# Optimization experiments

Measured on AMD Instinct MI355X. Metric: run time of the kernel, lower is better.

The kernel has to match this reference:

```python
import jax, jax.numpy as jnp
import numpy as np

B, T, D, H = 8, 2048, 1024, 128

def setup_inputs() -> dict:
    key = jax.random.key(0)
    ks = jax.random.split(key, 8)
    s = 1.0 / np.sqrt(D)
    return {
        "x": jax.random.normal(ks[0], (B, T, D), dtype=jnp.float32),
        "att": jax.random.normal(ks[1], (B, T, D), dtype=jnp.float32),
        "Wk": jax.random.uniform(ks[2], (D, H), minval=-s, maxval=s, dtype=jnp.float32),
        "bk": jax.random.uniform(ks[3], (H,), minval=-s, maxval=s, dtype=jnp.float32),
        "Wq": jax.random.uniform(ks[4], (D, H), minval=-s, maxval=s, dtype=jnp.float32),
        "bq": jax.random.uniform(ks[5], (H,), minval=-s, maxval=s, dtype=jnp.float32),
        "Wv": jax.random.uniform(ks[6], (D, H), minval=-s, maxval=s, dtype=jnp.float32),
        "bv": jax.random.uniform(ks[7], (H,), minval=-s, maxval=s, dtype=jnp.float32),
    }

def reference(x, att, Wk, bk, Wq, bq, Wv, bv):
    # k, q from `att`; v from `x` (as in the original module)
    k = jnp.einsum('btd,dh->bth', att, Wk) + bk   # [B,T,H]
    q = jnp.einsum('btd,dh->bth', att, Wq) + bq   # [B,T,H]
    v = jnp.einsum('btd,dh->bth', x, Wv) + bv     # [B,T,H]
    # Faithful to source: scores / head_size**(-0.5) == scores * sqrt(head_size)
    scale = jnp.asarray(k.shape[-1], jnp.float32) ** 0.5
    scores = jnp.einsum('bqh,bkh->bqk', q, k) * scale  # [B,T,T]
    att_mat = jax.nn.softmax(scores, axis=-1)
    # dropout p=0.0 -> identity (eval semantics)
    return jnp.einsum('bqk,bkh->bqh', att_mat, v)      # [B,T,H]
```

## Files before the change

### kernel.cpp

```cpp
#include <hip/hip_runtime.h>
#include <stdint.h>

typedef unsigned short u16;
typedef __attribute__((ext_vector_type(8))) short bf16x8;
typedef __attribute__((ext_vector_type(4))) float f32x4;

#define T_LEN 2048
#define D_DIM 1024
#define H_DIM 128
#define SCALE_LOG2 16.32223116f

#define EXP2F(x) __builtin_amdgcn_exp2f(x)

__device__ __forceinline__ u16 f2bf(float f) {
  uint32_t u = __float_as_uint(f);
  u += 0x7FFFu + ((u >> 16) & 1u);
  return (u16)(u >> 16);
}
__device__ __forceinline__ float bf2f(u16 h) { return __uint_as_float(((uint32_t)h) << 16); }

__device__ __forceinline__ void gload16(const void* g, void* l) {
  __builtin_amdgcn_global_load_lds(
      (const __attribute__((address_space(1))) uint32_t*)(uintptr_t)g,
      (__attribute__((address_space(3))) uint32_t*)(uint32_t)(uintptr_t)l,
      16, 0, 0);
}

#define MFMA(a, b, c) __builtin_amdgcn_mfma_f32_16x16x32_bf16((a), (b), (c), 0, 0, 0)

__global__ __launch_bounds__(256) void prep_w(
    const float* __restrict__ Wk, const float* __restrict__ Wq, const float* __restrict__ Wv,
    u16* __restrict__ wqh, u16* __restrict__ wql,
    u16* __restrict__ wkh, u16* __restrict__ wkl,
    u16* __restrict__ wvh) {
  __shared__ u16 th[3][128][16];
  __shared__ u16 tl[2][128][16];
  const int i = threadIdx.x;
  const int d0 = blockIdx.x * 16;
  const int dl = i >> 4;
  const int hb = (i & 15) * 8;
  const int d = d0 + dl;
#pragma unroll
  for (int e = 0; e < 8; ++e) {
    int h = hb + e;
    float q = Wq[d * H_DIM + h] * SCALE_LOG2;
    float k = Wk[d * H_DIM + h];
    float v = Wv[d * H_DIM + h];
    u16 qh = f2bf(q); th[0][h][dl] = qh; tl[0][h][dl] = f2bf(q - bf2f(qh));
    u16 kh = f2bf(k); th[1][h][dl] = kh; tl[1][h][dl] = f2bf(k - bf2f(kh));
    th[2][h][dl] = f2bf(v);
  }
  __syncthreads();
  const int h = i >> 1, c = i & 1;
  u16* planes[5] = {wqh, wql, wkh, wkl, wvh};
  const u16* srcs[5] = {&th[0][0][0], &tl[0][0][0], &th[1][0][0], &tl[1][0][0], &th[2][0][0]};
#pragma unroll
  for (int p = 0; p < 5; ++p) {
    bf16x8 v8 = *(const bf16x8*)(srcs[p] + h * 16 + c * 8);
    *(bf16x8*)(planes[p] + h * 1024 + d0 + c * 8) = v8;
  }
}

__global__ __launch_bounds__(256) void qkv_proj(
    const float* __restrict__ att, const float* __restrict__ x,
    const u16* __restrict__ wqh, const u16* __restrict__ wql,
    const u16* __restrict__ wkh, const u16* __restrict__ wkl,
    const u16* __restrict__ wvh,
    const float* __restrict__ bq, const float* __restrict__ bk, const float* __restrict__ bv,
    u16* __restrict__ qhp, u16* __restrict__ qlp,
    u16* __restrict__ khp, u16* __restrict__ klp,
    u16* __restrict__ vtp) {
  __shared__ __attribute__((aligned(128))) char lds[52 * 1024];
  char* aAh = lds;
  char* aAl = lds + 4096;
  char* aXh = lds + 8192;
  char* wt  = lds + 12288;
  char* vbuf = lds + 12288;

  const int tid = threadIdx.x;
  const int wid = tid >> 6;
  const int ln = tid & 63;
  const int g = ln >> 4;
  const int cl = ln & 15;
  const int t0g = blockIdx.x * 64;

  const f32x4 fz = {0.f, 0.f, 0.f, 0.f};
  f32x4 accq[2][4], acck[2][4], accv[2][4];
#pragma unroll
  for (int a = 0; a < 2; ++a)
#pragma unroll
    for (int s = 0; s < 4; ++s) { accq[a][s] = fz; acck[a][s] = fz; accv[a][s] = fz; }

  const int arow = tid >> 2;
  const int ac = tid & 3;
  const float* attp = att + (size_t)(t0g + arow) * D_DIM + ac * 8;
  const float* xp   = x   + (size_t)(t0g + arow) * D_DIM + ac * 8;
  char* aw = aAh + arow * 64 + ((ac ^ ((arow >> 1) & 3)) * 16);

  for (int ks = 0; ks < 32; ++ks) {
    __syncthreads();
    {
      f32x4 f0 = *(const f32x4*)(attp + ks * 32);
      f32x4 f1 = *(const f32x4*)(attp + ks * 32 + 4);
      f32x4 g0 = *(const f32x4*)(xp + ks * 32);
      f32x4 g1 = *(const f32x4*)(xp + ks * 32 + 4);
      bf16x8 vh, vl, vx;
#pragma unroll
      for (int e = 0; e < 4; ++e) {
        u16 h0 = f2bf(f0[e]); vh[e] = (short)h0; vl[e] = (short)f2bf(f0[e] - bf2f(h0));
        u16 h1 = f2bf(f1[e]); vh[e + 4] = (short)h1; vl[e + 4] = (short)f2bf(f1[e] - bf2f(h1));
        vx[e] = (short)f2bf(g0[e]); vx[e + 4] = (short)f2bf(g1[e]);
      }
      *(bf16x8*)aw = vh;
      *(bf16x8*)(aw + 4096) = vl;
      *(bf16x8*)(aw + 8192) = vx;
    }
#pragma unroll
    for (int j = 0; j < 10; ++j) {
      int seg = wid * 10 + j;
      int p = seg >> 3;
      int s = seg & 7;
      int db = s * 1024 + ln * 16;
      int row = db >> 6;
      int c = (db >> 4) & 3;
      int cs = c ^ ((row >> 1) & 3);
      const u16* wp = (p == 0) ? wqh : (p == 1) ? wql : (p == 2) ? wkh : (p == 3) ? wkl : wvh;
      gload16(wp + row * 1024 + ks * 32 + cs * 8, wt + p * 8192 + s * 1024);
    }
    __syncthreads();
    bf16x8 ah[4], al[4], xh[4];
#pragma unroll
    for (int s = 0; s < 4; ++s) {
      int row = s * 16 + cl;
      int byte = row * 64 + ((g ^ ((row >> 1) & 3)) * 16);
      ah[s] = *(const bf16x8*)(aAh + byte);
      al[s] = *(const bf16x8*)(aAl + byte);
      xh[s] = *(const bf16x8*)(aXh + byte);
    }
#pragma unroll
    for (int lnt = 0; lnt < 2; ++lnt) {
      int hrow = (2 * wid + lnt) * 16 + cl;
      int wb = hrow * 64 + ((g ^ ((hrow >> 1) & 3)) * 16);
      bf16x8 bqh_ = *(const bf16x8*)(wt + 0 * 8192 + wb);
      bf16x8 bql_ = *(const bf16x8*)(wt + 1 * 8192 + wb);
      bf16x8 bkh_ = *(const bf16x8*)(wt + 2 * 8192 + wb);
      bf16x8 bkl_ = *(const bf16x8*)(wt + 3 * 8192 + wb);
      bf16x8 bvh_ = *(const bf16x8*)(wt + 4 * 8192 + wb);
#pragma unroll
      for (int s = 0; s < 4; ++s) {
        accq[lnt][s] = MFMA(ah[s], bqh_, accq[lnt][s]);
        accq[lnt][s] = MFMA(al[s], bqh_, accq[lnt][s]);
        accq[lnt][s] = MFMA(ah[s], bql_, accq[lnt][s]);
        acck[lnt][s] = MFMA(ah[s], bkh_, acck[lnt][s]);
        acck[lnt][s] = MFMA(al[s], bkh_, acck[lnt][s]);
        acck[lnt][s] = MFMA(ah[s], bkl_, acck[lnt][s]);
        accv[lnt][s] = MFMA(xh[s], bvh_, accv[lnt][s]);
      }
    }
  }
  __syncthreads();
#pragma unroll
  for (int lnt = 0; lnt < 2; ++lnt) {
    int h = (2 * wid + lnt) * 16 + cl;
    float bqv = bq[h] * SCALE_LOG2, bkv = bk[h], bvv = bv[h];
#pragma unroll
    for (int s = 0; s < 4; ++s) {
#pragma unroll
      for (int r = 0; r < 4; ++r) {
        int t = s * 16 + g * 4 + r;
        size_t idx = (size_t)(t0g + t) * H_DIM + h;
        float qv = accq[lnt][s][r] + bqv;
        u16 qh_ = f2bf(qv);
        qhp[idx] = qh_;
        qlp[idx] = f2bf(qv - bf2f(qh_));
        float kv = acck[lnt][s][r] + bkv;
        u16 kh_ = f2bf(kv);
        khp[idx] = kh_;
        klp[idx] = f2bf(kv - bf2f(kh_));
        float vv = accv[lnt][s][r] + bvv;
        int c3 = t >> 3;
        int byte = h * 128 + ((c3 ^ (h & 7)) * 16) + (t & 7) * 2;
        *(u16*)(vbuf + byte) = f2bf(vv);
      }
    }
  }
  __syncthreads();
  {
    int h = tid >> 1, half = tid & 1;
    int b_ = t0g >> 11;
    int tb = t0g & 2047;
    u16* dst = vtp + ((size_t)(b_ * H_DIM + h)) * T_LEN + tb + half * 32;
#pragma unroll
    for (int c2 = 0; c2 < 4; ++c2) {
      int c3 = half * 4 + c2;
      bf16x8 v8 = *(const bf16x8*)(vbuf + h * 128 + ((c3 ^ (h & 7)) * 16));
      *(bf16x8*)(dst + c2 * 8) = v8;
    }
  }
}

__global__ __launch_bounds__(256) void attn(
    const u16* __restrict__ qhp, const u16* __restrict__ qlp,
    const u16* __restrict__ khp, const u16* __restrict__ klp,
    const u16* __restrict__ vtp,
    float* __restrict__ out) {
  __shared__ __attribute__((aligned(128))) char lds[56 * 1024];
  char* kH = lds;
  char* kL = lds + 16384;
  char* vT = lds + 32768;
  char* pB = lds + 49152;

  const int tid = threadIdx.x;
  const int wid = tid >> 6;
  const int ln = tid & 63;
  const int g = ln >> 4;
  const int cl = ln & 15;
  const int b_ = blockIdx.y;
  const int t0 = blockIdx.x * 64;
  char* pW = pB + wid * 2048;

  bf16x8 qh_f[4], ql_f[4];
  {
    size_t qrow = (size_t)(b_ * T_LEN + t0 + wid * 16 + cl) * H_DIM;
#pragma unroll
    for (int kc = 0; kc < 4; ++kc) {
      qh_f[kc] = *(const bf16x8*)(qhp + qrow + kc * 32 + g * 8);
      ql_f[kc] = *(const bf16x8*)(qlp + qrow + kc * 32 + g * 8);
    }
  }
  const f32x4 fz = {0.f, 0.f, 0.f, 0.f};
  float m_[4] = {-1e30f, -1e30f, -1e30f, -1e30f};
  float l_[4] = {0.f, 0.f, 0.f, 0.f};
  f32x4 o_[8];
#pragma unroll
  for (int ht = 0; ht < 8; ++ht) o_[ht] = fz;

  for (int kv = 0; kv < 32; ++kv) {
    const int tk = kv * 64;
    __syncthreads();
#pragma unroll
    for (int j = 0; j < 4; ++j) {
      int s = wid * 4 + j;
      int db = s * 1024 + ln * 16;
      int row = db >> 8;
      int c16 = (db >> 4) & 15;
      int cs = c16 ^ (row & 7);
      size_t gidx = (size_t)(b_ * T_LEN + tk + row) * H_DIM + cs * 8;
      gload16(khp + gidx, kH + s * 1024);
      gload16(klp + gidx, kL + s * 1024);
      int vrow = db >> 7;
      int c3 = (db >> 4) & 7;
      int vcs = c3 ^ (vrow & 7);
      size_t vidx = (size_t)(b_ * H_DIM + vrow) * T_LEN + tk + vcs * 8;
      gload16(vtp + vidx, vT + s * 1024);
    }
    __syncthreads();
    f32x4 sc[4];
#pragma unroll
    for (int nt = 0; nt < 4; ++nt) sc[nt] = fz;
#pragma unroll
    for (int kc = 0; kc < 4; ++kc) {
#pragma unroll
      for (int nt = 0; nt < 4; ++nt) {
        int row = nt * 16 + cl;
        int byte = row * 256 + (((kc * 4 + g) ^ (row & 7)) * 16);
        bf16x8 bh = *(const bf16x8*)(kH + byte);
        bf16x8 bl = *(const bf16x8*)(kL + byte);
        sc[nt] = MFMA(qh_f[kc], bh, sc[nt]);
        sc[nt] = MFMA(ql_f[kc], bh, sc[nt]);
        sc[nt] = MFMA(qh_f[kc], bl, sc[nt]);
      }
    }
    float sfv[4];
#pragma unroll
    for (int r = 0; r < 4; ++r) {
      float pm = fmaxf(fmaxf(sc[0][r], sc[1][r]), fmaxf(sc[2][r], sc[3][r]));
#pragma unroll
      for (int d = 1; d < 16; d <<= 1) pm = fmaxf(pm, __shfl_xor(pm, d));
      float mn = fmaxf(m_[r], pm);
      float sf = EXP2F(m_[r] - mn);
      m_[r] = mn; sfv[r] = sf;
      float ps = 0.f;
      int prow = g * 4 + r;
#pragma unroll
      for (int nt = 0; nt < 4; ++nt) {
        float p = EXP2F(sc[nt][r] - mn);
        ps += p;
        int c3 = nt * 2 + (cl >> 3);
        int byte = prow * 128 + ((c3 ^ (prow & 7)) * 16) + (cl & 7) * 2;
        *(u16*)(pW + byte) = f2bf(p);
      }
#pragma unroll
      for (int d = 1; d < 16; d <<= 1) ps += __shfl_xor(ps, d);
      l_[r] = l_[r] * sf + ps;
    }
#pragma unroll
    for (int ht = 0; ht < 8; ++ht) {
      o_[ht][0] *= sfv[0]; o_[ht][1] *= sfv[1]; o_[ht][2] *= sfv[2]; o_[ht][3] *= sfv[3];
    }
#pragma unroll
    for (int kc2 = 0; kc2 < 2; ++kc2) {
      int pbyte = cl * 128 + (((kc2 * 4 + g) ^ (cl & 7)) * 16);
      bf16x8 ap = *(const bf16x8*)(pW + pbyte);
#pragma unroll
      for (int ht = 0; ht < 8; ++ht) {
        int vrow = ht * 16 + cl;
        int vbyte = vrow * 128 + (((kc2 * 4 + g) ^ (vrow & 7)) * 16);
        bf16x8 bv_ = *(const bf16x8*)(vT + vbyte);
        o_[ht] = MFMA(ap, bv_, o_[ht]);
      }
    }
  }
  float inv[4];
#pragma unroll
  for (int r = 0; r < 4; ++r) inv[r] = 1.f / l_[r];
  size_t obase = (size_t)(b_ * T_LEN + t0 + wid * 16) * H_DIM;
#pragma unroll
  for (int r = 0; r < 4; ++r) {
#pragma unroll
    for (int ht = 0; ht < 8; ++ht) {
      out[obase + (size_t)(g * 4 + r) * H_DIM + ht * 16 + cl] = o_[ht][r] * inv[r];
    }
  }
}

extern "C" void kernel_launch(void* const* d_in, const int* in_sizes, int n_in,
                              void* d_out, int out_size, void* d_ws, size_t ws_size,
                              hipStream_t stream) {
  const float* x   = (const float*)d_in[0];
  const float* att = (const float*)d_in[1];
  const float* Wk  = (const float*)d_in[2];
  const float* bk  = (const float*)d_in[3];
  const float* Wq  = (const float*)d_in[4];
  const float* bq  = (const float*)d_in[5];
  const float* Wv  = (const float*)d_in[6];
  const float* bv  = (const float*)d_in[7];
  float* out = (float*)d_out;
  char* ws = (char*)d_ws;

  u16* wqh = (u16*)(ws);
  u16* wql = (u16*)(ws + 256 * 1024);
  u16* wkh = (u16*)(ws + 512 * 1024);
  u16* wkl = (u16*)(ws + 768 * 1024);
  u16* wvh = (u16*)(ws + 1024 * 1024);
  u16* qhp = (u16*)(ws + (size_t)2 * 1024 * 1024);
  u16* qlp = (u16*)(ws + (size_t)6 * 1024 * 1024);
  u16* khp = (u16*)(ws + (size_t)10 * 1024 * 1024);
  u16* klp = (u16*)(ws + (size_t)14 * 1024 * 1024);
  u16* vtp = (u16*)(ws + (size_t)18 * 1024 * 1024);

  prep_w<<<64, 256, 0, stream>>>(Wk, Wq, Wv, wqh, wql, wkh, wkl, wvh);
  qkv_proj<<<256, 256, 0, stream>>>(att, x, wqh, wql, wkh, wkl, wvh,
                                    bq, bk, bv, qhp, qlp, khp, klp, vtp);
  attn<<<dim3(32, 8), 256, 0, stream>>>(qhp, qlp, khp, klp, vtp, out);
}
```

Measured before the change: 309.1 us.

## Double-buffer LDS staging in projection and attention kernels to overlap loads

Both qkv_proj and attn now use two LDS buffers. The next K-slice of weights and activations (or the next K/V tile) is issued while MFMAs run on the current one, and the two barriers per iteration become one. This hides global-load latency behind compute. The attention grid is also flattened and reordered so consecutive blocks hit different batches. In exchange LDS per block grows to 104KB, which likely limits each CU to one block and reduces occupancy.

```diff
diff --git a/kernel.cpp b/kernel.cpp
--- a/kernel.cpp
+++ b/kernel.cpp
@@ -25,6 +25,10 @@
       (__attribute__((address_space(3))) uint32_t*)(uint32_t)(uintptr_t)l,
       16, 0, 0);
 }
+
+#define VMCNT0() asm volatile("s_waitcnt vmcnt(0)" ::: "memory")
+#define VMLG0() asm volatile("s_waitcnt vmcnt(0) lgkmcnt(0)" ::: "memory")
+#define BAR() __builtin_amdgcn_s_barrier()
 
 #define MFMA(a, b, c) __builtin_amdgcn_mfma_f32_16x16x32_bf16((a), (b), (c), 0, 0, 0)
 
@@ -61,6 +65,8 @@
   }
 }
 
+#define QBUF 53248
+
 __global__ __launch_bounds__(256) void qkv_proj(
     const float* __restrict__ att, const float* __restrict__ x,
     const u16* __restrict__ wqh, const u16* __restrict__ wql,
@@ -70,12 +76,7 @@
     u16* __restrict__ qhp, u16* __restrict__ qlp,
     u16* __restrict__ khp, u16* __restrict__ klp,
     u16* __restrict__ vtp) {
-  __shared__ __attribute__((aligned(128))) char lds[52 * 1024];
-  char* aAh = lds;
-  char* aAl = lds + 4096;
-  char* aXh = lds + 8192;
-  char* wt  = lds + 12288;
-  char* vbuf = lds + 12288;
+  __shared__ __attribute__((aligned(128))) char lds[104 * 1024];
 
   const int tid = threadIdx.x;
   const int wid = tid >> 6;
@@ -95,26 +96,10 @@
   const int ac = tid & 3;
   const float* attp = att + (size_t)(t0g + arow) * D_DIM + ac * 8;
   const float* xp   = x   + (size_t)(t0g + arow) * D_DIM + ac * 8;
-  char* aw = aAh + arow * 64 + ((ac ^ ((arow >> 1) & 3)) * 16);
-
-  for (int ks = 0; ks < 32; ++ks) {
-    __syncthreads();
-    {
-      f32x4 f0 = *(const f32x4*)(attp + ks * 32);
-      f32x4 f1 = *(const f32x4*)(attp + ks * 32 + 4);
-      f32x4 g0 = *(const f32x4*)(xp + ks * 32);
-      f32x4 g1 = *(const f32x4*)(xp + ks * 32 + 4);
-      bf16x8 vh, vl, vx;
-#pragma unroll
-      for (int e = 0; e < 4; ++e) {
-        u16 h0 = f2bf(f0[e]); vh[e] = (short)h0; vl[e] = (short)f2bf(f0[e] - bf2f(h0));
-        u16 h1 = f2bf(f1[e]); vh[e + 4] = (short)h1; vl[e + 4] = (short)f2bf(f1[e] - bf2f(h1));
-        vx[e] = (short)f2bf(g0[e]); vx[e + 4] = (short)f2bf(g1[e]);
-      }
-      *(bf16x8*)aw = vh;
-      *(bf16x8*)(aw + 4096) = vl;
-      *(bf16x8*)(aw + 8192) = vx;
-    }
+  const int aw_off = arow * 64 + ((ac ^ ((arow >> 1) & 3)) * 16);
+
+  auto STAGE_W = [&](int b, int ks) {
+    char* wt = lds + b * QBUF + 12288;
 #pragma unroll
     for (int j = 0; j < 10; ++j) {
       int seg = wid * 10 + j;
@@ -127,7 +112,47 @@
       const u16* wp = (p == 0) ? wqh : (p == 1) ? wql : (p == 2) ? wkh : (p == 3) ? wkl : wvh;
       gload16(wp + row * 1024 + ks * 32 + cs * 8, wt + p * 8192 + s * 1024);
     }
-    __syncthreads();
+  };
+  auto CWRITE_A = [&](int b, f32x4 f0, f32x4 f1, f32x4 g0, f32x4 g1) {
+    bf16x8 vh, vl, vx;
+#pragma unroll
+    for (int e = 0; e < 4; ++e) {
+      u16 h0 = f2bf(f0[e]); vh[e] = (short)h0; vl[e] = (short)f2bf(f0[e] - bf2f(h0));
+      u16 h1 = f2bf(f1[e]); vh[e + 4] = (short)h1; vl[e + 4] = (short)f2bf(f1[e] - bf2f(h1));
+      vx[e] = (short)f2bf(g0[e]); vx[e + 4] = (short)f2bf(g1[e]);
+    }
+    char* dst = lds + b * QBUF + aw_off;
+    *(bf16x8*)dst = vh;
+    *(bf16x8*)(dst + 4096) = vl;
+    *(bf16x8*)(dst + 8192) = vx;
+  };
+
+  {
+    f32x4 f0 = *(const f32x4*)(attp);
+    f32x4 f1 = *(const f32x4*)(attp + 4);
+    f32x4 g0 = *(const f32x4*)(xp);
+    f32x4 g1 = *(const f32x4*)(xp + 4);
+    STAGE_W(0, 0);
+    CWRITE_A(0, f0, f1, g0, g1);
+  }
+  VMLG0();
+  BAR();
+
+  int cur = 0;
+  for (int ks = 0; ks < 32; ++ks) {
+    f32x4 pf0, pf1, pg0, pg1;
+    if (ks < 31) {
+      pf0 = *(const f32x4*)(attp + (ks + 1) * 32);
+      pf1 = *(const f32x4*)(attp + (ks + 1) * 32 + 4);
+      pg0 = *(const f32x4*)(xp + (ks + 1) * 32);
+      pg1 = *(const f32x4*)(xp + (ks + 1) * 32 + 4);
+      STAGE_W(cur ^ 1, ks + 1);
+    }
+    char* base = lds + cur * QBUF;
+    char* aAh = base;
+    char* aAl = base + 4096;
+    char* aXh = base + 8192;
+    char* wt  = base + 12288;
     bf16x8 ah[4], al[4], xh[4];
 #pragma unroll
     for (int s = 0; s < 4; ++s) {
@@ -157,8 +182,13 @@
         accv[lnt][s] = MFMA(xh[s], bvh_, accv[lnt][s]);
       }
     }
-  }
-  __syncthreads();
+    if (ks < 31) CWRITE_A(cur ^ 1, pf0, pf1, pg0, pg1);
+    VMLG0();
+    BAR();
+    cur ^= 1;
+  }
+
+  char* vbuf = lds;
 #pragma unroll
   for (int lnt = 0; lnt < 2; ++lnt) {
     int h = (2 * wid + lnt) * 16 + cl;
@@ -199,45 +229,30 @@
   }
 }
 
+#define ABUF 49152
+
 __global__ __launch_bounds__(256) void attn(
     const u16* __restrict__ qhp, const u16* __restrict__ qlp,
     const u16* __restrict__ khp, const u16* __restrict__ klp,
     const u16* __restrict__ vtp,
     float* __restrict__ out) {
-  __shared__ __attribute__((aligned(128))) char lds[56 * 1024];
-  char* kH = lds;
-  char* kL = lds + 16384;
-  char* vT = lds + 32768;
-  char* pB = lds + 49152;
+  __shared__ __attribute__((aligned(128))) char lds[104 * 1024];
+  char* pB = lds + 96 * 1024;
 
   const int tid = threadIdx.x;
   const int wid = tid >> 6;
   const int ln = tid & 63;
   const int g = ln >> 4;
   const int cl = ln & 15;
-  const int b_ = blockIdx.y;
-  const int t0 = blockIdx.x * 64;
+  const int bid = blockIdx.x;
+  const int b_ = bid & 7;
+  const int t0 = (bid >> 3) * 64;
   char* pW = pB + wid * 2048;
 
-  bf16x8 qh_f[4], ql_f[4];
-  {
-    size_t qrow = (size_t)(b_ * T_LEN + t0 + wid * 16 + cl) * H_DIM;
-#pragma unroll
-    for (int kc = 0; kc < 4; ++kc) {
-      qh_f[kc] = *(const bf16x8*)(qhp + qrow + kc * 32 + g * 8);
-      ql_f[kc] = *(const bf16x8*)(qlp + qrow + kc * 32 + g * 8);
-    }
-  }
-  const f32x4 fz = {0.f, 0.f, 0.f, 0.f};
-  float m_[4] = {-1e30f, -1e30f, -1e30f, -1e30f};
-  float l_[4] = {0.f, 0.f, 0.f, 0.f};
-  f32x4 o_[8];
-#pragma unroll
-  for (int ht = 0; ht < 8; ++ht) o_[ht] = fz;
-
-  for (int kv = 0; kv < 32; ++kv) {
-    const int tk = kv * 64;
-    __syncthreads();
+  auto STAGE = [&](int b, int tk) {
+    char* kH = lds + b * ABUF;
+    char* kL = kH + 16384;
+    char* vT = kH + 32768;
 #pragma unroll
     for (int j = 0; j < 4; ++j) {
       int s = wid * 4 + j;
@@ -254,7 +269,35 @@
       size_t vidx = (size_t)(b_ * H_DIM + vrow) * T_LEN + tk + vcs * 8;
       gload16(vtp + vidx, vT + s * 1024);
     }
-    __syncthreads();
+  };
+
+  bf16x8 qh_f[4], ql_f[4];
+  {
+    size_t qrow = (size_t)(b_ * T_LEN + t0 + wid * 16 + cl) * H_DIM;
+#pragma unroll
+    for (int kc = 0; kc < 4; ++kc) {
+      qh_f[kc] = *(const bf16x8*)(qhp + qrow + kc * 32 + g * 8);
+      ql_f[kc] = *(const bf16x8*)(qlp + qrow + kc * 32 + g * 8);
+    }
+  }
+  const f32x4 fz = {0.f, 0.f, 0.f, 0.f};
+  float m_[4] = {-1e30f, -1e30f, -1e30f, -1e30f};
+  float l_[4] = {0.f, 0.f, 0.f, 0.f};
+  f32x4 o_[8];
+#pragma unroll
+  for (int ht = 0; ht < 8; ++ht) o_[ht] = fz;
+
+  STAGE(0, 0);
+  VMCNT0();
+  BAR();
+
+  int cur = 0;
+  for (int kv = 0; kv < 32; ++kv) {
+    if (kv < 31) STAGE(cur ^ 1, (kv + 1) * 64);
+
+    char* kH = lds + cur * ABUF;
+    char* kL = kH + 16384;
+    char* vT = kH + 32768;
     f32x4 sc[4];
 #pragma unroll
     for (int nt = 0; nt < 4; ++nt) sc[nt] = fz;
@@ -310,6 +353,9 @@
         o_[ht] = MFMA(ap, bv_, o_[ht]);
       }
     }
+    VMCNT0();
+    BAR();
+    cur ^= 1;
   }
   float inv[4];
 #pragma unroll
@@ -352,5 +398,5 @@
   prep_w<<<64, 256, 0, stream>>>(Wk, Wq, Wv, wqh, wql, wkh, wkl, wvh);
   qkv_proj<<<256, 256, 0, stream>>>(att, x, wqh, wql, wkh, wkl, wvh,
                                     bq, bk, bv, qhp, qlp, khp, klp, vtp);
-  attn<<<dim3(32, 8), 256, 0, stream>>>(qhp, qlp, khp, klp, vtp, out);
-}
+  attn<<<256, 256, 0, stream>>>(qhp, qlp, khp, klp, vtp, out);
+}
```

Measured after the change: 265.2 us. 1.17x faster.
